# Kernel tuning notes

Hardware: AMD Instinct MI355X
Metric: run time of the kernel (lower is better)

## Reference

```python
import jax, jax.numpy as jnp
import numpy as np

N_NODES = 50000
N_EDGES = 800000
IN_FEATS = 128
HIDDEN = 64
EDGE_FEATS = 3


def setup_inputs() -> dict:
    key = jax.random.key(0)
    ks = jax.random.split(key, 8)
    s = lambda d: 1.0 / np.sqrt(d)
    return {
        "x": jax.random.normal(ks[0], (N_NODES, IN_FEATS), jnp.float32),
        "efeat": jax.random.normal(ks[1], (N_EDGES, EDGE_FEATS), jnp.float32),
        "src": jax.random.randint(ks[2], (N_EDGES,), 0, N_NODES, jnp.int32),
        "dst": jax.random.randint(ks[3], (N_EDGES,), 0, N_NODES, jnp.int32),
        "W1": jax.random.normal(ks[4], (IN_FEATS, HIDDEN), jnp.float32) * s(IN_FEATS),
        "b1": jnp.zeros((HIDDEN,), jnp.float32),
        "W2": jax.random.normal(ks[5], (HIDDEN, HIDDEN), jnp.float32) * s(HIDDEN),
        "b2": jnp.zeros((HIDDEN,), jnp.float32),
        "We": jax.random.normal(ks[6], (2 * HIDDEN + EDGE_FEATS, 1), jnp.float32) * s(2 * HIDDEN + EDGE_FEATS),
        "be": jnp.zeros((1,), jnp.float32),
    }


def reference(x, efeat, src, dst, W1, b1, W2, b2, We, be):
    n = x.shape[0]
    ones = jnp.ones(src.shape[0], x.dtype)
    # DGL GraphConv norm='both': scale src feats by out-deg^-1/2, aggregate, scale by in-deg^-1/2
    deg_out = jnp.clip(jax.ops.segment_sum(ones, src, num_segments=n), 1.0)
    deg_in = jnp.clip(jax.ops.segment_sum(ones, dst, num_segments=n), 1.0)
    c_src = deg_out ** -0.5  # [N]
    c_dst = deg_in ** -0.5   # [N]

    def graph_conv(h, W, b):
        hn = h * c_src[:, None]                             # pre-scale
        agg = jax.ops.segment_sum(hn[src], dst, num_segments=n)
        return (agg * c_dst[:, None]) @ W + b

    h = jax.nn.relu(graph_conv(x, W1, b1))
    h = graph_conv(h, W2, b2)

    # edge_func: sigmoid(Linear(cat[src_h, dst_h, efeat])) -- split We to avoid concat
    H = h.shape[1]
    Ws, Wd, Wf = We[:H], We[H:2 * H], We[2 * H:]
    logits = h[src] @ Ws + h[dst] @ Wd + efeat @ Wf + be   # [E, 1]
    return jax.nn.sigmoid(logits[:, 0])                    # [E]
```

## Files before the change

### kernel.cpp

```cpp
#include <hip/hip_runtime.h>
#include <math.h>
#include <stdint.h>

#define N_NODES 50000
#define N_EDGES 800000
#define IN_FEATS 128
#define HIDDEN 64

#define CSPLIT 32
#define CHUNK (N_EDGES / CSPLIT)
#define NQUART (N_NODES / 4)
#define NQWORDS (NQUART / 2)

#define NB_E4 782
#define NB_GEMM 782

typedef __attribute__((ext_vector_type(8))) short bf16x8;
typedef __attribute__((ext_vector_type(4))) float f32x4;

__device__ __forceinline__ unsigned short f2bf(float f) {
    unsigned u = __float_as_uint(f);
    u = (u + 0x7FFF + ((u >> 16) & 1)) >> 16;
    return (unsigned short)u;
}

#define ACC8(A, r)                                \
    A[0] += __uint_as_float((r).x << 16);         \
    A[1] += __uint_as_float((r).x & 0xffff0000u); \
    A[2] += __uint_as_float((r).y << 16);         \
    A[3] += __uint_as_float((r).y & 0xffff0000u); \
    A[4] += __uint_as_float((r).z << 16);         \
    A[5] += __uint_as_float((r).z & 0xffff0000u); \
    A[6] += __uint_as_float((r).w << 16);         \
    A[7] += __uint_as_float((r).w & 0xffff0000u);

__global__ __launch_bounds__(256) void hist2_kernel(const int* __restrict__ src,
                                                    const int* __restrict__ dst,
                                                    unsigned short* __restrict__ epos,
                                                    unsigned* __restrict__ pin,
                                                    unsigned* __restrict__ pout) {
    __shared__ unsigned cnt[NQWORDS];
    int b = blockIdx.x;
    int c = b >> 3;
    int kind = (b >> 2) & 1;
    int quar = b & 3;
    int lo = quar * NQUART;
    for (int i = threadIdx.x; i < NQWORDS; i += 256) cnt[i] = 0;
    __syncthreads();
    if (kind == 0) {
        const int4* d4 = reinterpret_cast<const int4*>(dst + c * CHUNK);
        for (int i = threadIdx.x; i < CHUNK / 4; i += 256) {
            int4 d = d4[i];
            int e = c * CHUNK + i * 4;
            unsigned u, old;
            u = (unsigned)(d.x - lo);
            if (u < NQUART) { old = atomicAdd(&cnt[u >> 1], 1u << ((u & 1) * 16));
                              epos[e + 0] = (unsigned short)(old >> ((u & 1) * 16)); }
            u = (unsigned)(d.y - lo);
            if (u < NQUART) { old = atomicAdd(&cnt[u >> 1], 1u << ((u & 1) * 16));
                              epos[e + 1] = (unsigned short)(old >> ((u & 1) * 16)); }
            u = (unsigned)(d.z - lo);
            if (u < NQUART) { old = atomicAdd(&cnt[u >> 1], 1u << ((u & 1) * 16));
                              epos[e + 2] = (unsigned short)(old >> ((u & 1) * 16)); }
            u = (unsigned)(d.w - lo);
            if (u < NQUART) { old = atomicAdd(&cnt[u >> 1], 1u << ((u & 1) * 16));
                              epos[e + 3] = (unsigned short)(old >> ((u & 1) * 16)); }
        }
    } else {
        const int4* s4 = reinterpret_cast<const int4*>(src + c * CHUNK);
        for (int i = threadIdx.x; i < CHUNK / 4; i += 256) {
            int4 s = s4[i];
            unsigned u;
            u = (unsigned)(s.x - lo); if (u < NQUART) atomicAdd(&cnt[u >> 1], 1u << ((u & 1) * 16));
            u = (unsigned)(s.y - lo); if (u < NQUART) atomicAdd(&cnt[u >> 1], 1u << ((u & 1) * 16));
            u = (unsigned)(s.z - lo); if (u < NQUART) atomicAdd(&cnt[u >> 1], 1u << ((u & 1) * 16));
            u = (unsigned)(s.w - lo); if (u < NQUART) atomicAdd(&cnt[u >> 1], 1u << ((u & 1) * 16));
        }
    }
    __syncthreads();
    unsigned* outp = (kind ? pout : pin) + c * (N_NODES / 2) + quar * NQWORDS;
    for (int i = threadIdx.x; i < NQWORDS; i += 256) outp[i] = cnt[i];
}

__global__ __launch_bounds__(256) void prep_kernel(const unsigned* __restrict__ pin,
                                                   const unsigned* __restrict__ pout,
                                                   float* __restrict__ cs,
                                                   float* __restrict__ cd,
                                                   int* __restrict__ offs,
                                                   int* __restrict__ bsum,
                                                   const float* __restrict__ W2,
                                                   const float* __restrict__ We,
                                                   const float* __restrict__ b2,
                                                   float* __restrict__ w2s,
                                                   float* __restrict__ w2d,
                                                   float* __restrict__ w2c) {
    int b = blockIdx.x;
    int t = threadIdx.x;
    if (b == 49) {
        if (t < 64) {
            float s = 0.f, d = 0.f;
            for (int j = 0; j < HIDDEN; ++j) {
                float w = W2[t * HIDDEN + j];
                s = fmaf(w, We[j], s);
                d = fmaf(w, We[HIDDEN + j], d);
            }
            w2s[t] = s;
            w2d[t] = d;
        } else if (t == 64) {
            float s = 0.f, d = 0.f;
            for (int j = 0; j < HIDDEN; ++j) {
                s = fmaf(We[j], b2[j], s);
                d = fmaf(We[HIDDEN + j], b2[j], d);
            }
            w2c[0] = s;
            w2c[1] = d;
        }
        return;
    }
    __shared__ int sums[256];
    int v0 = b * 1024 + t * 4;
    bool ok = v0 < N_NODES;
    unsigned si0 = 0, si1 = 0, si2 = 0, si3 = 0;
    unsigned so0 = 0, so1 = 0, so2 = 0, so3 = 0;
    if (ok) {
        int w0 = v0 >> 1;
#pragma unroll
        for (int c = 0; c < CSPLIT; ++c) {
            uint2 a = *reinterpret_cast<const uint2*>(pin + (size_t)c * (N_NODES / 2) + w0);
            uint2 o = *reinterpret_cast<const uint2*>(pout + (size_t)c * (N_NODES / 2) + w0);
            si0 += a.x & 0xffffu; si1 += a.x >> 16;
            si2 += a.y & 0xffffu; si3 += a.y >> 16;
            so0 += o.x & 0xffffu; so1 += o.x >> 16;
            so2 += o.y & 0xffffu; so3 += o.y >> 16;
        }
        *reinterpret_cast<float4*>(cs + v0) =
            make_float4(rsqrtf(fmaxf((float)so0, 1.f)), rsqrtf(fmaxf((float)so1, 1.f)),
                        rsqrtf(fmaxf((float)so2, 1.f)), rsqrtf(fmaxf((float)so3, 1.f)));
        *reinterpret_cast<float4*>(cd + v0) =
            make_float4(rsqrtf(fmaxf((float)si0, 1.f)), rsqrtf(fmaxf((float)si1, 1.f)),
                        rsqrtf(fmaxf((float)si2, 1.f)), rsqrtf(fmaxf((float)si3, 1.f)));
    }
    int d0 = (int)si0, d1 = (int)si1, d2 = (int)si2, d3 = (int)si3;
    sums[t] = d0 + d1 + d2 + d3;
    __syncthreads();
    for (int o = 1; o < 256; o <<= 1) {
        int v = (t >= o) ? sums[t - o] : 0;
        __syncthreads();
        sums[t] += v;
        __syncthreads();
    }
    int excl = (t == 0) ? 0 : sums[t - 1];
    if (ok) {
        *reinterpret_cast<int4*>(offs + v0) =
            make_int4(excl, excl + d0, excl + d0 + d1, excl + d0 + d1 + d2);
    }
    if (t == 255) bsum[b] = sums[255];
}

__global__ __launch_bounds__(256) void scan3_base_kernel(int* __restrict__ offs,
                                                         const int* __restrict__ bsum,
                                                         const unsigned* __restrict__ pin,
                                                         unsigned short* __restrict__ baser) {
    __shared__ int sbase[64];
    int t = threadIdx.x;
    if (t < 64) {
        int val = (t < 49) ? bsum[t] : 0;
        int s = val;
#pragma unroll
        for (int o = 1; o < 64; o <<= 1) {
            int u = __shfl_up(s, o, 64);
            if (t >= o) s += u;
        }
        sbase[t] = s - val;
    }
    __syncthreads();
    int v = blockIdx.x * 256 + t;
    if (v >= N_NODES) return;
    int off = offs[v] + sbase[v >> 10];
    offs[v] = off;
    int rel = 0;
    int sh = (v & 1) * 16;
#pragma unroll
    for (int c = 0; c < CSPLIT; ++c) {
        baser[(size_t)c * N_NODES + v] = (unsigned short)rel;
        rel += (int)((pin[(size_t)c * (N_NODES / 2) + (v >> 1)] >> sh) & 0xffffu);
    }
    if (v == 0) offs[N_NODES] = N_EDGES;
}

__global__ __launch_bounds__(256) void fill_gemm_kernel(const int* __restrict__ src,
                                                        const int* __restrict__ dst,
                                                        const unsigned short* __restrict__ epos,
                                                        const int* __restrict__ offs,
                                                        const unsigned short* __restrict__ baser,
                                                        int* __restrict__ csr_src,
                                                        const float* __restrict__ x,
                                                        const float* __restrict__ c_src,
                                                        const float* __restrict__ W,
                                                        unsigned short* __restrict__ yb) {
    __shared__ bf16x8 Bfrag[16][64];
    if (blockIdx.x < NB_E4) {
        int t = blockIdx.x * 256 + threadIdx.x;
        int e0 = t * 4;
        if (e0 >= N_EDGES) return;
        int c = e0 / CHUNK;
        const unsigned short* brc = baser + (size_t)c * N_NODES;
        int4 s = *reinterpret_cast<const int4*>(src + e0);
        int4 d = *reinterpret_cast<const int4*>(dst + e0);
        ushort4 ep = *reinterpret_cast<const ushort4*>(epos + e0);
        csr_src[offs[d.x] + brc[d.x] + ep.x] = s.x;
        csr_src[offs[d.y] + brc[d.y] + ep.y] = s.y;
        csr_src[offs[d.z] + brc[d.z] + ep.z] = s.z;
        csr_src[offs[d.w] + brc[d.w] + ep.w] = s.w;
        return;
    }
    int gb = blockIdx.x - NB_E4;
    for (int idx = threadIdx.x; idx < 16 * 64; idx += 256) {
        int f = idx >> 6, l = idx & 63;
        int nt = f >> 2, kt = f & 3;
        int col = nt * 16 + (l & 15);
        int k0 = kt * 32 + (l >> 4) * 8;
        bf16x8 bv;
#pragma unroll
        for (int j = 0; j < 8; ++j) bv[j] = (short)f2bf(W[(k0 + j) * HIDDEN + col]);
        Bfrag[f][l] = bv;
    }
    __syncthreads();
    int wid = threadIdx.x >> 6, l = threadIdx.x & 63;
    bf16x8 Breg[16];
#pragma unroll
    for (int f = 0; f < 16; ++f) Breg[f] = Bfrag[f][l];

    int row0 = gb * 64 + wid * 16;
    int arow = row0 + (l & 15);
    int asafe = min(arow, N_NODES - 1);
    const float* xr = x + (size_t)asafe * IN_FEATS + (l >> 4) * 8;
    f32x4 acc0 = {0.f, 0.f, 0.f, 0.f};
    f32x4 acc1 = {0.f, 0.f, 0.f, 0.f};
    f32x4 acc2 = {0.f, 0.f, 0.f, 0.f};
    f32x4 acc3 = {0.f, 0.f, 0.f, 0.f};
#pragma unroll
    for (int kt = 0; kt < 4; ++kt) {
        float4 a0 = *reinterpret_cast<const float4*>(xr + kt * 32);
        float4 a1 = *reinterpret_cast<const float4*>(xr + kt * 32 + 4);
        bf16x8 av;
        av[0] = (short)f2bf(a0.x); av[1] = (short)f2bf(a0.y);
        av[2] = (short)f2bf(a0.z); av[3] = (short)f2bf(a0.w);
        av[4] = (short)f2bf(a1.x); av[5] = (short)f2bf(a1.y);
        av[6] = (short)f2bf(a1.z); av[7] = (short)f2bf(a1.w);
        acc0 = __builtin_amdgcn_mfma_f32_16x16x32_bf16(av, Breg[0 * 4 + kt], acc0, 0, 0, 0);
        acc1 = __builtin_amdgcn_mfma_f32_16x16x32_bf16(av, Breg[1 * 4 + kt], acc1, 0, 0, 0);
        acc2 = __builtin_amdgcn_mfma_f32_16x16x32_bf16(av, Breg[2 * 4 + kt], acc2, 0, 0, 0);
        acc3 = __builtin_amdgcn_mfma_f32_16x16x32_bf16(av, Breg[3 * 4 + kt], acc3, 0, 0, 0);
    }
#pragma unroll
    for (int i = 0; i < 4; ++i) {
        int row = row0 + (l >> 4) * 4 + i;
        if (row < N_NODES) {
            float cs = c_src[row];
            unsigned short* yr = yb + (size_t)row * HIDDEN + (l & 15);
            yr[0]  = f2bf(acc0[i] * cs);
            yr[16] = f2bf(acc1[i] * cs);
            yr[32] = f2bf(acc2[i] * cs);
            yr[48] = f2bf(acc3[i] * cs);
        }
    }
}

__global__ __launch_bounds__(256) void gather_t_kernel(const unsigned short* __restrict__ y,
                                                       const int* __restrict__ offs,
                                                       const int* __restrict__ csr_src,
                                                       const float* __restrict__ c_src,
                                                       const float* __restrict__ c_dst,
                                                       const float* __restrict__ b1,
                                                       const float* __restrict__ w2s,
                                                       const float* __restrict__ w2d,
                                                       float2* __restrict__ t) {
    int wid = threadIdx.x >> 6, l = threadIdx.x & 63;
    int slot = l >> 3, q8 = l & 7;
    int v0 = blockIdx.x * 8 + wid * 2;
    int v1 = v0 + 1;
    int beg0 = offs[v0], end0 = offs[v0 + 1], end1 = offs[v0 + 2];
    int k0 = beg0, k1 = end0;
    float acc0[8] = {0.f, 0.f, 0.f, 0.f, 0.f, 0.f, 0.f, 0.f};
    float acc1[8] = {0.f, 0.f, 0.f, 0.f, 0.f, 0.f, 0.f, 0.f};
    while (k0 + 8 <= end0 && k1 + 8 <= end1) {
        int sA = csr_src[k0 + slot];
        int sB = csr_src[k1 + slot];
        uint4 rA = *reinterpret_cast<const uint4*>(y + (size_t)sA * HIDDEN + q8 * 8);
        uint4 rB = *reinterpret_cast<const uint4*>(y + (size_t)sB * HIDDEN + q8 * 8);
        ACC8(acc0, rA);
        ACC8(acc1, rB);
        k0 += 8;
        k1 += 8;
    }
    while (k0 + 8 <= end0) {
        int s = csr_src[k0 + slot];
        uint4 r = *reinterpret_cast<const uint4*>(y + (size_t)s * HIDDEN + q8 * 8);
        ACC8(acc0, r);
        k0 += 8;
    }
    while (k1 + 8 <= end1) {
        int s = csr_src[k1 + slot];
        uint4 r = *reinterpret_cast<const uint4*>(y + (size_t)s * HIDDEN + q8 * 8);
        ACC8(acc1, r);
        k1 += 8;
    }
    if (slot < end0 - k0) {
        int s = csr_src[k0 + slot];
        uint4 r = *reinterpret_cast<const uint4*>(y + (size_t)s * HIDDEN + q8 * 8);
        ACC8(acc0, r);
    }
    if (slot < end1 - k1) {
        int s = csr_src[k1 + slot];
        uint4 r = *reinterpret_cast<const uint4*>(y + (size_t)s * HIDDEN + q8 * 8);
        ACC8(acc1, r);
    }
#pragma unroll
    for (int i = 0; i < 8; ++i) {
        acc0[i] += __shfl_xor(acc0[i], 8, 64);
        acc0[i] += __shfl_xor(acc0[i], 16, 64);
        acc0[i] += __shfl_xor(acc0[i], 32, 64);
        acc1[i] += __shfl_xor(acc1[i], 8, 64);
        acc1[i] += __shfl_xor(acc1[i], 16, 64);
        acc1[i] += __shfl_xor(acc1[i], 32, 64);
    }
    float4 ba = *reinterpret_cast<const float4*>(b1 + q8 * 8);
    float4 bb = *reinterpret_cast<const float4*>(b1 + q8 * 8 + 4);
    float4 wsa = *reinterpret_cast<const float4*>(w2s + q8 * 8);
    float4 wsb = *reinterpret_cast<const float4*>(w2s + q8 * 8 + 4);
    float4 wda = *reinterpret_cast<const float4*>(w2d + q8 * 8);
    float4 wdb = *reinterpret_cast<const float4*>(w2d + q8 * 8 + 4);
    float c0 = c_dst[v0], c1 = c_dst[v1];
    float h0, h1, h2, h3, h4, h5, h6, h7;
    h0 = fmaxf(fmaf(c0, acc0[0], ba.x), 0.f);
    h1 = fmaxf(fmaf(c0, acc0[1], ba.y), 0.f);
    h2 = fmaxf(fmaf(c0, acc0[2], ba.z), 0.f);
    h3 = fmaxf(fmaf(c0, acc0[3], ba.w), 0.f);
    h4 = fmaxf(fmaf(c0, acc0[4], bb.x), 0.f);
    h5 = fmaxf(fmaf(c0, acc0[5], bb.y), 0.f);
    h6 = fmaxf(fmaf(c0, acc0[6], bb.z), 0.f);
    h7 = fmaxf(fmaf(c0, acc0[7], bb.w), 0.f);
    float ps0 = h0 * wsa.x + h1 * wsa.y + h2 * wsa.z + h3 * wsa.w
              + h4 * wsb.x + h5 * wsb.y + h6 * wsb.z + h7 * wsb.w;
    float pd0 = h0 * wda.x + h1 * wda.y + h2 * wda.z + h3 * wda.w
              + h4 * wdb.x + h5 * wdb.y + h6 * wdb.z + h7 * wdb.w;
    h0 = fmaxf(fmaf(c1, acc1[0], ba.x), 0.f);
    h1 = fmaxf(fmaf(c1, acc1[1], ba.y), 0.f);
    h2 = fmaxf(fmaf(c1, acc1[2], ba.z), 0.f);
    h3 = fmaxf(fmaf(c1, acc1[3], ba.w), 0.f);
    h4 = fmaxf(fmaf(c1, acc1[4], bb.x), 0.f);
    h5 = fmaxf(fmaf(c1, acc1[5], bb.y), 0.f);
    h6 = fmaxf(fmaf(c1, acc1[6], bb.z), 0.f);
    h7 = fmaxf(fmaf(c1, acc1[7], bb.w), 0.f);
    float ps1 = h0 * wsa.x + h1 * wsa.y + h2 * wsa.z + h3 * wsa.w
              + h4 * wsb.x + h5 * wsb.y + h6 * wsb.z + h7 * wsb.w;
    float pd1 = h0 * wda.x + h1 * wda.y + h2 * wda.z + h3 * wda.w
              + h4 * wdb.x + h5 * wdb.y + h6 * wdb.z + h7 * wdb.w;
#pragma unroll
    for (int o = 1; o <= 4; o <<= 1) {
        ps0 += __shfl_xor(ps0, o, 64);
        pd0 += __shfl_xor(pd0, o, 64);
        ps1 += __shfl_xor(ps1, o, 64);
        pd1 += __shfl_xor(pd1, o, 64);
    }
    if (l == 0) {
        float cs0 = c_src[v0], cs1 = c_src[v1];
        *reinterpret_cast<float4*>(t + v0) =
            make_float4(cs0 * ps0, cs0 * pd0, cs1 * ps1, cs1 * pd1);
    }
}

__global__ __launch_bounds__(256) void gather2_kernel(const float2* __restrict__ t,
                                                      const int* __restrict__ offs,
                                                      const int* __restrict__ csr_src,
                                                      const float* __restrict__ c_dst,
                                                      const float* __restrict__ w2c,
                                                      float* __restrict__ a_s,
                                                      float* __restrict__ a_d) {
    int wid = threadIdx.x >> 6, l = threadIdx.x & 63;
    int sub = l >> 4, q = l & 15;
    int v = blockIdx.x * 16 + wid * 4 + sub;
    int beg = offs[v], end = offs[v + 1];
    float ps = 0.f, pd = 0.f;
    for (int k = beg + q; k < end; k += 16) {
        float2 tv = t[csr_src[k]];
        ps += tv.x;
        pd += tv.y;
    }
#pragma unroll
    for (int o = 1; o <= 8; o <<= 1) {
        ps += __shfl_xor(ps, o, 64);
        pd += __shfl_xor(pd, o, 64);
    }
    if (q == 0) {
        float c = c_dst[v];
        a_s[v] = fmaf(c, ps, w2c[0]);
        a_d[v] = fmaf(c, pd, w2c[1]);
    }
}

__global__ __launch_bounds__(256) void edge_out_kernel(const int* __restrict__ src,
                                                       const int* __restrict__ dst,
                                                       const float* __restrict__ efeat,
                                                       const float* __restrict__ We,
                                                       const float* __restrict__ be,
                                                       const float* __restrict__ a_s,
                                                       const float* __restrict__ a_d,
                                                       float* __restrict__ out) {
    int t = blockIdx.x * 256 + threadIdx.x;
    int e0 = t * 8;
    if (e0 >= N_EDGES) return;
    float w0 = We[2 * HIDDEN + 0], w1 = We[2 * HIDDEN + 1], w2 = We[2 * HIDDEN + 2];
    float b = be[0];
    int4 sA = *reinterpret_cast<const int4*>(src + e0);
    int4 sB = *reinterpret_cast<const int4*>(src + e0 + 4);
    int4 dA = *reinterpret_cast<const int4*>(dst + e0);
    int4 dB = *reinterpret_cast<const int4*>(dst + e0 + 4);
    const float4* f = reinterpret_cast<const float4*>(efeat + (long)e0 * 3);
    float4 f0 = f[0], f1 = f[1], f2 = f[2], f3 = f[3], f4 = f[4], f5 = f[5];
    float as0 = a_s[sA.x], as1 = a_s[sA.y], as2 = a_s[sA.z], as3 = a_s[sA.w];
    float as4 = a_s[sB.x], as5 = a_s[sB.y], as6 = a_s[sB.z], as7 = a_s[sB.w];
    float ad0 = a_d[dA.x], ad1 = a_d[dA.y], ad2 = a_d[dA.z], ad3 = a_d[dA.w];
    float ad4 = a_d[dB.x], ad5 = a_d[dB.y], ad6 = a_d[dB.z], ad7 = a_d[dB.w];
    float4 oA, oB;
    float z;
    z = as0 + ad0 + f0.x * w0 + f0.y * w1 + f0.z * w2 + b;
    oA.x = 1.0f / (1.0f + __expf(-z));
    z = as1 + ad1 + f0.w * w0 + f1.x * w1 + f1.y * w2 + b;
    oA.y = 1.0f / (1.0f + __expf(-z));
    z = as2 + ad2 + f1.z * w0 + f1.w * w1 + f2.x * w2 + b;
    oA.z = 1.0f / (1.0f + __expf(-z));
    z = as3 + ad3 + f2.y * w0 + f2.z * w1 + f2.w * w2 + b;
    oA.w = 1.0f / (1.0f + __expf(-z));
    z = as4 + ad4 + f3.x * w0 + f3.y * w1 + f3.z * w2 + b;
    oB.x = 1.0f / (1.0f + __expf(-z));
    z = as5 + ad5 + f3.w * w0 + f4.x * w1 + f4.y * w2 + b;
    oB.y = 1.0f / (1.0f + __expf(-z));
    z = as6 + ad6 + f4.z * w0 + f4.w * w1 + f5.x * w2 + b;
    oB.z = 1.0f / (1.0f + __expf(-z));
    z = as7 + ad7 + f5.y * w0 + f5.z * w1 + f5.w * w2 + b;
    oB.w = 1.0f / (1.0f + __expf(-z));
    *reinterpret_cast<float4*>(out + e0) = oA;
    *reinterpret_cast<float4*>(out + e0 + 4) = oB;
}

extern "C" void kernel_launch(void* const* d_in, const int* in_sizes, int n_in,
                              void* d_out, int out_size, void* d_ws, size_t ws_size,
                              hipStream_t stream) {
    const float* x     = (const float*)d_in[0];
    const float* efeat = (const float*)d_in[1];
    const int*   src   = (const int*)d_in[2];
    const int*   dst   = (const int*)d_in[3];
    const float* W1    = (const float*)d_in[4];
    const float* b1    = (const float*)d_in[5];
    const float* W2    = (const float*)d_in[6];
    const float* b2    = (const float*)d_in[7];
    const float* We    = (const float*)d_in[8];
    const float* be    = (const float*)d_in[9];
    float* out = (float*)d_out;

    char* p = (char*)d_ws;
    auto alloc = [&](size_t bytes) {
        char* r = p;
        p += (bytes + 255) & ~(size_t)255;
        return r;
    };
    float* c_src   = (float*)alloc((size_t)N_NODES * 4);
    float* c_dst   = (float*)alloc((size_t)N_NODES * 4);
    float* a_s     = (float*)alloc((size_t)N_NODES * 4);
    float* a_d     = (float*)alloc((size_t)N_NODES * 4);
    int*   offs    = (int*)alloc((size_t)(N_NODES + 1) * 4);
    int*   bsum    = (int*)alloc(64 * 4);
    float* w2s     = (float*)alloc(HIDDEN * 4);
    float* w2d     = (float*)alloc(HIDDEN * 4);
    float* w2c     = (float*)alloc(2 * 4);
    unsigned*       pin   = (unsigned*)alloc((size_t)CSPLIT * (N_NODES / 2) * 4);
    unsigned*       pout  = (unsigned*)alloc((size_t)CSPLIT * (N_NODES / 2) * 4);
    unsigned short* epos  = (unsigned short*)alloc((size_t)N_EDGES * 2);
    unsigned short* baser = (unsigned short*)alloc((size_t)CSPLIT * N_NODES * 2);
    int*            csr_src = (int*)alloc((size_t)N_EDGES * 4);
    unsigned short* yb    = (unsigned short*)alloc((size_t)N_NODES * HIDDEN * 2);
    float2*         t     = (float2*)alloc((size_t)N_NODES * 8);

    const int NB_V = (N_NODES + 255) / 256;

    hist2_kernel<<<CSPLIT * 8, 256, 0, stream>>>(src, dst, epos, pin, pout);
    prep_kernel<<<50, 256, 0, stream>>>(pin, pout, c_src, c_dst, offs, bsum,
                                        W2, We, b2, w2s, w2d, w2c);
    scan3_base_kernel<<<NB_V, 256, 0, stream>>>(offs, bsum, pin, baser);

    fill_gemm_kernel<<<NB_E4 + NB_GEMM, 256, 0, stream>>>(src, dst, epos, offs, baser,
                                                          csr_src, x, c_src, W1, yb);

    gather_t_kernel<<<N_NODES / 8, 256, 0, stream>>>(yb, offs, csr_src, c_src, c_dst,
                                                     b1, w2s, w2d, t);

    gather2_kernel<<<N_NODES / 16, 256, 0, stream>>>(t, offs, csr_src, c_dst, w2c, a_s, a_d);

    edge_out_kernel<<<(N_EDGES / 8 + 255) / 256, 256, 0, stream>>>(src, dst, efeat, We, be,
                                                                   a_s, a_d, out);
}
```

Measured before the change: 97.40 us.

## Move X·W1 GEMM into histogram kernel and apply source norm in gather

The dense X·W1 GEMM no longer waits for degree normalisation. It now runs in the same launch as the degree histogram, sharing LDS through a union, so the matrix-core work overlaps the atomic-bound histogram. The c_src scaling moves into the gather as an FMA with a per-edge load of c_src[s], which adds one extra random load per edge. The fill kernel becomes a standalone launch.

```diff
diff --git a/kernel.cpp b/kernel.cpp
--- a/kernel.cpp
+++ b/kernel.cpp
@@ -12,6 +12,7 @@
 #define NQUART (N_NODES / 4)
 #define NQWORDS (NQUART / 2)
 
+#define NB_HIST 256
 #define NB_E4 782
 #define NB_GEMM 782
 
@@ -24,62 +25,121 @@
     return (unsigned short)u;
 }
 
-#define ACC8(A, r)                                \
-    A[0] += __uint_as_float((r).x << 16);         \
-    A[1] += __uint_as_float((r).x & 0xffff0000u); \
-    A[2] += __uint_as_float((r).y << 16);         \
-    A[3] += __uint_as_float((r).y & 0xffff0000u); \
-    A[4] += __uint_as_float((r).z << 16);         \
-    A[5] += __uint_as_float((r).z & 0xffff0000u); \
-    A[6] += __uint_as_float((r).w << 16);         \
-    A[7] += __uint_as_float((r).w & 0xffff0000u);
-
-__global__ __launch_bounds__(256) void hist2_kernel(const int* __restrict__ src,
-                                                    const int* __restrict__ dst,
-                                                    unsigned short* __restrict__ epos,
-                                                    unsigned* __restrict__ pin,
-                                                    unsigned* __restrict__ pout) {
-    __shared__ unsigned cnt[NQWORDS];
-    int b = blockIdx.x;
-    int c = b >> 3;
-    int kind = (b >> 2) & 1;
-    int quar = b & 3;
-    int lo = quar * NQUART;
-    for (int i = threadIdx.x; i < NQWORDS; i += 256) cnt[i] = 0;
+#define ACC8F(A, r, cs)                                        \
+    A[0] = fmaf(cs, __uint_as_float((r).x << 16), A[0]);       \
+    A[1] = fmaf(cs, __uint_as_float((r).x & 0xffff0000u), A[1]); \
+    A[2] = fmaf(cs, __uint_as_float((r).y << 16), A[2]);       \
+    A[3] = fmaf(cs, __uint_as_float((r).y & 0xffff0000u), A[3]); \
+    A[4] = fmaf(cs, __uint_as_float((r).z << 16), A[4]);       \
+    A[5] = fmaf(cs, __uint_as_float((r).z & 0xffff0000u), A[5]); \
+    A[6] = fmaf(cs, __uint_as_float((r).w << 16), A[6]);       \
+    A[7] = fmaf(cs, __uint_as_float((r).w & 0xffff0000u), A[7]);
+
+__global__ __launch_bounds__(256) void hist_gemm_kernel(const int* __restrict__ src,
+                                                        const int* __restrict__ dst,
+                                                        unsigned short* __restrict__ epos,
+                                                        unsigned* __restrict__ pin,
+                                                        unsigned* __restrict__ pout,
+                                                        const float* __restrict__ x,
+                                                        const float* __restrict__ W,
+                                                        unsigned short* __restrict__ yb) {
+    __shared__ union {
+        unsigned cnt[NQWORDS];
+        bf16x8 bfrag[16][64];
+    } u;
+    if (blockIdx.x < NB_HIST) {
+        int b = blockIdx.x;
+        int c = b >> 3;
+        int kind = (b >> 2) & 1;
+        int quar = b & 3;
+        int lo = quar * NQUART;
+        for (int i = threadIdx.x; i < NQWORDS; i += 256) u.cnt[i] = 0;
+        __syncthreads();
+        if (kind == 0) {
+            const int4* d4 = reinterpret_cast<const int4*>(dst + c * CHUNK);
+            for (int i = threadIdx.x; i < CHUNK / 4; i += 256) {
+                int4 d = d4[i];
+                int e = c * CHUNK + i * 4;
+                unsigned q, old;
+                q = (unsigned)(d.x - lo);
+                if (q < NQUART) { old = atomicAdd(&u.cnt[q >> 1], 1u << ((q & 1) * 16));
+                                  epos[e + 0] = (unsigned short)(old >> ((q & 1) * 16)); }
+                q = (unsigned)(d.y - lo);
+                if (q < NQUART) { old = atomicAdd(&u.cnt[q >> 1], 1u << ((q & 1) * 16));
+                                  epos[e + 1] = (unsigned short)(old >> ((q & 1) * 16)); }
+                q = (unsigned)(d.z - lo);
+                if (q < NQUART) { old = atomicAdd(&u.cnt[q >> 1], 1u << ((q & 1) * 16));
+                                  epos[e + 2] = (unsigned short)(old >> ((q & 1) * 16)); }
+                q = (unsigned)(d.w - lo);
+                if (q < NQUART) { old = atomicAdd(&u.cnt[q >> 1], 1u << ((q & 1) * 16));
+                                  epos[e + 3] = (unsigned short)(old >> ((q & 1) * 16)); }
+            }
+        } else {
+            const int4* s4 = reinterpret_cast<const int4*>(src + c * CHUNK);
+            for (int i = threadIdx.x; i < CHUNK / 4; i += 256) {
+                int4 s = s4[i];
+                unsigned q;
+                q = (unsigned)(s.x - lo); if (q < NQUART) atomicAdd(&u.cnt[q >> 1], 1u << ((q & 1) * 16));
+                q = (unsigned)(s.y - lo); if (q < NQUART) atomicAdd(&u.cnt[q >> 1], 1u << ((q & 1) * 16));
+                q = (unsigned)(s.z - lo); if (q < NQUART) atomicAdd(&u.cnt[q >> 1], 1u << ((q & 1) * 16));
+                q = (unsigned)(s.w - lo); if (q < NQUART) atomicAdd(&u.cnt[q >> 1], 1u << ((q & 1) * 16));
+            }
+        }
+        __syncthreads();
+        unsigned* outp = (kind ? pout : pin) + c * (N_NODES / 2) + quar * NQWORDS;
+        for (int i = threadIdx.x; i < NQWORDS; i += 256) outp[i] = u.cnt[i];
+        return;
+    }
+    int gb = blockIdx.x - NB_HIST;
+    for (int idx = threadIdx.x; idx < 16 * 64; idx += 256) {
+        int f = idx >> 6, l = idx & 63;
+        int nt = f >> 2, kt = f & 3;
+        int col = nt * 16 + (l & 15);
+        int k0 = kt * 32 + (l >> 4) * 8;
+        bf16x8 bv;
+#pragma unroll
+        for (int j = 0; j < 8; ++j) bv[j] = (short)f2bf(W[(k0 + j) * HIDDEN + col]);
+        u.bfrag[f][l] = bv;
+    }
     __syncthreads();
-    if (kind == 0) {
-        const int4* d4 = reinterpret_cast<const int4*>(dst + c * CHUNK);
-        for (int i = threadIdx.x; i < CHUNK / 4; i += 256) {
-            int4 d = d4[i];
-            int e = c * CHUNK + i * 4;
-            unsigned u, old;
-            u = (unsigned)(d.x - lo);
-            if (u < NQUART) { old = atomicAdd(&cnt[u >> 1], 1u << ((u & 1) * 16));
-                              epos[e + 0] = (unsigned short)(old >> ((u & 1) * 16)); }
-            u = (unsigned)(d.y - lo);
-            if (u < NQUART) { old = atomicAdd(&cnt[u >> 1], 1u << ((u & 1) * 16));
-                              epos[e + 1] = (unsigned short)(old >> ((u & 1) * 16)); }
-            u = (unsigned)(d.z - lo);
-            if (u < NQUART) { old = atomicAdd(&cnt[u >> 1], 1u << ((u & 1) * 16));
-                              epos[e + 2] = (unsigned short)(old >> ((u & 1) * 16)); }
-            u = (unsigned)(d.w - lo);
-            if (u < NQUART) { old = atomicAdd(&cnt[u >> 1], 1u << ((u & 1) * 16));
-                              epos[e + 3] = (unsigned short)(old >> ((u & 1) * 16)); }
+    int wid = threadIdx.x >> 6, l = threadIdx.x & 63;
+    bf16x8 Breg[16];
+#pragma unroll
+    for (int f = 0; f < 16; ++f) Breg[f] = u.bfrag[f][l];
+
+    int row0 = gb * 64 + wid * 16;
+    int arow = row0 + (l & 15);
+    int asafe = min(arow, N_NODES - 1);
+    const float* xr = x + (size_t)asafe * IN_FEATS + (l >> 4) * 8;
+    f32x4 acc0 = {0.f, 0.f, 0.f, 0.f};
+    f32x4 acc1 = {0.f, 0.f, 0.f, 0.f};
+    f32x4 acc2 = {0.f, 0.f, 0.f, 0.f};
+    f32x4 acc3 = {0.f, 0.f, 0.f, 0.f};
+#pragma unroll
+    for (int kt = 0; kt < 4; ++kt) {
+        float4 a0 = *reinterpret_cast<const float4*>(xr + kt * 32);
+        float4 a1 = *reinterpret_cast<const float4*>(xr + kt * 32 + 4);
+        bf16x8 av;
+        av[0] = (short)f2bf(a0.x); av[1] = (short)f2bf(a0.y);
+        av[2] = (short)f2bf(a0.z); av[3] = (short)f2bf(a0.w);
+        av[4] = (short)f2bf(a1.x); av[5] = (short)f2bf(a1.y);
+        av[6] = (short)f2bf(a1.z); av[7] = (short)f2bf(a1.w);
+        acc0 = __builtin_amdgcn_mfma_f32_16x16x32_bf16(av, Breg[0 * 4 + kt], acc0, 0, 0, 0);
+        acc1 = __builtin_amdgcn_mfma_f32_16x16x32_bf16(av, Breg[1 * 4 + kt], acc1, 0, 0, 0);
+        acc2 = __builtin_amdgcn_mfma_f32_16x16x32_bf16(av, Breg[2 * 4 + kt], acc2, 0, 0, 0);
+        acc3 = __builtin_amdgcn_mfma_f32_16x16x32_bf16(av, Breg[3 * 4 + kt], acc3, 0, 0, 0);
+    }
+#pragma unroll
+    for (int i = 0; i < 4; ++i) {
+        int row = row0 + (l >> 4) * 4 + i;
+        if (row < N_NODES) {
+            unsigned short* yr = yb + (size_t)row * HIDDEN + (l & 15);
+            yr[0]  = f2bf(acc0[i]);
+            yr[16] = f2bf(acc1[i]);
+            yr[32] = f2bf(acc2[i]);
+            yr[48] = f2bf(acc3[i]);
         }
-    } else {
-        const int4* s4 = reinterpret_cast<const int4*>(src + c * CHUNK);
-        for (int i = threadIdx.x; i < CHUNK / 4; i += 256) {
-            int4 s = s4[i];
-            unsigned u;
-            u = (unsigned)(s.x - lo); if (u < NQUART) atomicAdd(&cnt[u >> 1], 1u << ((u & 1) * 16));
-            u = (unsigned)(s.y - lo); if (u < NQUART) atomicAdd(&cnt[u >> 1], 1u << ((u & 1) * 16));
-            u = (unsigned)(s.z - lo); if (u < NQUART) atomicAdd(&cnt[u >> 1], 1u << ((u & 1) * 16));
-            u = (unsigned)(s.w - lo); if (u < NQUART) atomicAdd(&cnt[u >> 1], 1u << ((u & 1) * 16));
-        }
-    }
-    __syncthreads();
-    unsigned* outp = (kind ? pout : pin) + c * (N_NODES / 2) + quar * NQWORDS;
-    for (int i = threadIdx.x; i < NQWORDS; i += 256) outp[i] = cnt[i];
+    }
 }
 
 __global__ __launch_bounds__(256) void prep_kernel(const unsigned* __restrict__ pin,
@@ -188,83 +248,24 @@
     if (v == 0) offs[N_NODES] = N_EDGES;
 }
 
-__global__ __launch_bounds__(256) void fill_gemm_kernel(const int* __restrict__ src,
-                                                        const int* __restrict__ dst,
-                                                        const unsigned short* __restrict__ epos,
-                                                        const int* __restrict__ offs,
-                                                        const unsigned short* __restrict__ baser,
-                                                        int* __restrict__ csr_src,
-                                                        const float* __restrict__ x,
-                                                        const float* __restrict__ c_src,
-                                                        const float* __restrict__ W,
-                                                        unsigned short* __restrict__ yb) {
-    __shared__ bf16x8 Bfrag[16][64];
-    if (blockIdx.x < NB_E4) {
-        int t = blockIdx.x * 256 + threadIdx.x;
-        int e0 = t * 4;
-        if (e0 >= N_EDGES) return;
-        int c = e0 / CHUNK;
-        const unsigned short* brc = baser + (size_t)c * N_NODES;
-        int4 s = *reinterpret_cast<const int4*>(src + e0);
-        int4 d = *reinterpret_cast<const int4*>(dst + e0);
-        ushort4 ep = *reinterpret_cast<const ushort4*>(epos + e0);
-        csr_src[offs[d.x] + brc[d.x] + ep.x] = s.x;
-        csr_src[offs[d.y] + brc[d.y] + ep.y] = s.y;
-        csr_src[offs[d.z] + brc[d.z] + ep.z] = s.z;
-        csr_src[offs[d.w] + brc[d.w] + ep.w] = s.w;
-        return;
-    }
-    int gb = blockIdx.x - NB_E4;
-    for (int idx = threadIdx.x; idx < 16 * 64; idx += 256) {
-        int f = idx >> 6, l = idx & 63;
-        int nt = f >> 2, kt = f & 3;
-        int col = nt * 16 + (l & 15);
-        int k0 = kt * 32 + (l >> 4) * 8;
-        bf16x8 bv;
-#pragma unroll
-        for (int j = 0; j < 8; ++j) bv[j] = (short)f2bf(W[(k0 + j) * HIDDEN + col]);
-        Bfrag[f][l] = bv;
-    }
-    __syncthreads();
-    int wid = threadIdx.x >> 6, l = threadIdx.x & 63;
-    bf16x8 Breg[16];
-#pragma unroll
-    for (int f = 0; f < 16; ++f) Breg[f] = Bfrag[f][l];
-
-    int row0 = gb * 64 + wid * 16;
-    int arow = row0 + (l & 15);
-    int asafe = min(arow, N_NODES - 1);
-    const float* xr = x + (size_t)asafe * IN_FEATS + (l >> 4) * 8;
-    f32x4 acc0 = {0.f, 0.f, 0.f, 0.f};
-    f32x4 acc1 = {0.f, 0.f, 0.f, 0.f};
-    f32x4 acc2 = {0.f, 0.f, 0.f, 0.f};
-    f32x4 acc3 = {0.f, 0.f, 0.f, 0.f};
-#pragma unroll
-    for (int kt = 0; kt < 4; ++kt) {
-        float4 a0 = *reinterpret_cast<const float4*>(xr + kt * 32);
-        float4 a1 = *reinterpret_cast<const float4*>(xr + kt * 32 + 4);
-        bf16x8 av;
-        av[0] = (short)f2bf(a0.x); av[1] = (short)f2bf(a0.y);
-        av[2] = (short)f2bf(a0.z); av[3] = (short)f2bf(a0.w);
-        av[4] = (short)f2bf(a1.x); av[5] = (short)f2bf(a1.y);
-        av[6] = (short)f2bf(a1.z); av[7] = (short)f2bf(a1.w);
-        acc0 = __builtin_amdgcn_mfma_f32_16x16x32_bf16(av, Breg[0 * 4 + kt], acc0, 0, 0, 0);
-        acc1 = __builtin_amdgcn_mfma_f32_16x16x32_bf16(av, Breg[1 * 4 + kt], acc1, 0, 0, 0);
-        acc2 = __builtin_amdgcn_mfma_f32_16x16x32_bf16(av, Breg[2 * 4 + kt], acc2, 0, 0, 0);
-        acc3 = __builtin_amdgcn_mfma_f32_16x16x32_bf16(av, Breg[3 * 4 + kt], acc3, 0, 0, 0);
-    }
-#pragma unroll
-    for (int i = 0; i < 4; ++i) {
-        int row = row0 + (l >> 4) * 4 + i;
-        if (row < N_NODES) {
-            float cs = c_src[row];
-            unsigned short* yr = yb + (size_t)row * HIDDEN + (l & 15);
-            yr[0]  = f2bf(acc0[i] * cs);
-            yr[16] = f2bf(acc1[i] * cs);
-            yr[32] = f2bf(acc2[i] * cs);
-            yr[48] = f2bf(acc3[i] * cs);
-        }
-    }
+__global__ __launch_bounds__(256) void fill_kernel(const int* __restrict__ src,
+                                                   const int* __restrict__ dst,
+                                                   const unsigned short* __restrict__ epos,
+                                                   const int* __restrict__ offs,
+                                                   const unsigned short* __restrict__ baser,
+                                                   int* __restrict__ csr_src) {
+    int t = blockIdx.x * 256 + threadIdx.x;
+    int e0 = t * 4;
+    if (e0 >= N_EDGES) return;
+    int c = e0 / CHUNK;
+    const unsigned short* brc = baser + (size_t)c * N_NODES;
+    int4 s = *reinterpret_cast<const int4*>(src + e0);
+    int4 d = *reinterpret_cast<const int4*>(dst + e0);
+    ushort4 ep = *reinterpret_cast<const ushort4*>(epos + e0);
+    csr_src[offs[d.x] + brc[d.x] + ep.x] = s.x;
+    csr_src[offs[d.y] + brc[d.y] + ep.y] = s.y;
+    csr_src[offs[d.z] + brc[d.z] + ep.z] = s.z;
+    csr_src[offs[d.w] + brc[d.w] + ep.w] = s.w;
 }
 
 __global__ __launch_bounds__(256) void gather_t_kernel(const unsigned short* __restrict__ y,
@@ -287,34 +288,40 @@
     while (k0 + 8 <= end0 && k1 + 8 <= end1) {
         int sA = csr_src[k0 + slot];
         int sB = csr_src[k1 + slot];
+        float csA = c_src[sA];
+        float csB = c_src[sB];
         uint4 rA = *reinterpret_cast<const uint4*>(y + (size_t)sA * HIDDEN + q8 * 8);
         uint4 rB = *reinterpret_cast<const uint4*>(y + (size_t)sB * HIDDEN + q8 * 8);
-        ACC8(acc0, rA);
-        ACC8(acc1, rB);
+        ACC8F(acc0, rA, csA);
+        ACC8F(acc1, rB, csB);
         k0 += 8;
         k1 += 8;
     }
     while (k0 + 8 <= end0) {
         int s = csr_src[k0 + slot];
+        float cs = c_src[s];
         uint4 r = *reinterpret_cast<const uint4*>(y + (size_t)s * HIDDEN + q8 * 8);
-        ACC8(acc0, r);
+        ACC8F(acc0, r, cs);
         k0 += 8;
     }
     while (k1 + 8 <= end1) {
         int s = csr_src[k1 + slot];
+        float cs = c_src[s];
         uint4 r = *reinterpret_cast<const uint4*>(y + (size_t)s * HIDDEN + q8 * 8);
-        ACC8(acc1, r);
+        ACC8F(acc1, r, cs);
         k1 += 8;
     }
     if (slot < end0 - k0) {
         int s = csr_src[k0 + slot];
+        float cs = c_src[s];
         uint4 r = *reinterpret_cast<const uint4*>(y + (size_t)s * HIDDEN + q8 * 8);
-        ACC8(acc0, r);
+        ACC8F(acc0, r, cs);
     }
     if (slot < end1 - k1) {
         int s = csr_src[k1 + slot];
+        float cs = c_src[s];
         uint4 r = *reinterpret_cast<const uint4*>(y + (size_t)s * HIDDEN + q8 * 8);
-        ACC8(acc1, r);
+        ACC8F(acc1, r, cs);
     }
 #pragma unroll
     for (int i = 0; i < 8; ++i) {
@@ -485,19 +492,15 @@
 
     const int NB_V = (N_NODES + 255) / 256;
 
-    hist2_kernel<<<CSPLIT * 8, 256, 0, stream>>>(src, dst, epos, pin, pout);
+    hist_gemm_kernel<<<NB_HIST + NB_GEMM, 256, 0, stream>>>(src, dst, epos, pin, pout,
+                                                            x, W1, yb);
     prep_kernel<<<50, 256, 0, stream>>>(pin, pout, c_src, c_dst, offs, bsum,
                                         W2, We, b2, w2s, w2d, w2c);
     scan3_base_kernel<<<NB_V, 256, 0, stream>>>(offs, bsum, pin, baser);
-
-    fill_gemm_kernel<<<NB_E4 + NB_GEMM, 256, 0, stream>>>(src, dst, epos, offs, baser,
-                                                          csr_src, x, c_src, W1, yb);
-
+    fill_kernel<<<NB_E4, 256, 0, stream>>>(src, dst, epos, offs, baser, csr_src);
     gather_t_kernel<<<N_NODES / 8, 256, 0, stream>>>(yb, offs, csr_src, c_src, c_dst,
                                                      b1, w2s, w2d, t);
-
     gather2_kernel<<<N_NODES / 16, 256, 0, stream>>>(t, offs, csr_src, c_dst, w2c, a_s, a_d);
-
     edge_out_kernel<<<(N_EDGES / 8 + 255) / 256, 256, 0, stream>>>(src, dst, efeat, We, be,
                                                                    a_s, a_d, out);
 }
```

After: 93.53 us, median of 2. -4.0%, faster.
